# Performance work log

Hardware: AMD Instinct MI355X
Metric: run time of the kernel (lower is better)

## Reference

```python
import jax, jax.numpy as jnp
import numpy as np

NUM_LABELS = 64
START, END, PAD = 0, 1, 2
B, L, V, D = 128, 1024, 30000, 256


def make_transitions(key):
    # replicates CRF.init_weights
    t = jax.random.uniform(key, (NUM_LABELS, NUM_LABELS), minval=-0.1, maxval=0.1)
    t = t.at[:, START].set(-10000.0)
    t = t.at[END, :].set(-10000.0)
    t = t.at[PAD, :].set(-10000.0)
    t = t.at[:, PAD].set(-10000.0)
    t = t.at[PAD, PAD].set(0.0)
    t = t.at[PAD, END].set(0.0)
    return t.astype(jnp.float32)


def setup_inputs() -> dict:
    key = jax.random.key(0)
    k0, k1, k2, k3, k4 = jax.random.split(key, 5)
    x = jax.random.randint(k0, (B, L), 0, V)
    tags = jax.random.randint(k1, (B, L), 0, NUM_LABELS)
    mask = jnp.ones((B, L), dtype=jnp.float32)  # ignored by CRF (source passes mask=None)
    embed = jax.random.normal(k2, (V, D), dtype=jnp.float32)
    W = jax.random.normal(k3, (D, NUM_LABELS), dtype=jnp.float32) * 0.05
    b = jnp.zeros((NUM_LABELS,), dtype=jnp.float32)
    trans = make_transitions(k4)
    return {"x": x, "tags": tags, "mask": mask, "embed": embed, "W": W, "b": b, "trans": trans}


def _crf_nll(emissions, tags, trans):
    # emissions: [B, L, T]; tags: [B, L]; trans: [T, T]
    # NOTE: original CRF.forward ignores the user mask (passes mask=None ->
    # all-ones mask), so every position is valid and last tag is tags[:, -1].
    # gold path score
    e_scores = jnp.take_along_axis(emissions, tags[:, :, None], axis=2)[:, :, 0].sum(axis=1)
    t_scores = trans[tags[:, :-1], tags[:, 1:]].sum(axis=1)
    scores = e_scores + t_scores + trans[START, tags[:, 0]] + trans[tags[:, -1], END]
    # log partition: forward algorithm (log-space recursion over time)
    alpha0 = trans[START][None, :] + emissions[:, 0]  # [B, T]

    def step(alphas, emit_t):
        # alphas: [B, T_prev] -> logsumexp over previous tag
        new = jax.nn.logsumexp(alphas[:, :, None] + trans[None, :, :], axis=1) + emit_t
        return new, None

    alphas, _ = jax.lax.scan(step, alpha0, jnp.swapaxes(emissions[:, 1:], 0, 1))
    log_z = jax.nn.logsumexp(alphas + trans[:, END][None, :], axis=1)  # [B]
    return -jnp.sum(scores - log_z)


def reference(x, tags, mask, embed, W, b, trans):
    emissions = embed[x] @ W + b  # [B, L, T]
    return _crf_nll(emissions, tags, trans)
```

## Files before the change

kernel.cpp:

```cpp
#include <hip/hip_runtime.h>
#include <hip/hip_bf16.h>

#define B_ 128
#define L_ 1024
#define T_ 64
#define CSH 5
#define C_ 32

using short8 = __attribute__((ext_vector_type(8))) short;
using f32x4  = __attribute__((ext_vector_type(4))) float;
using f32x16 = __attribute__((ext_vector_type(16))) float;

static __device__ __forceinline__ unsigned short bfb(float x) {
  return __builtin_bit_cast(unsigned short, __float2bfloat16(x));
}
static __device__ __forceinline__ float asf(unsigned u) { return __builtin_bit_cast(float, u); }
static __device__ __forceinline__ float bf2f(unsigned short b) { return asf(((unsigned)b) << 16); }
static __device__ __forceinline__ unsigned pk2(float lo, float hi) {
  __hip_bfloat162 h = __float22bfloat162_rn(float2{lo, hi});
  unsigned u;
  __builtin_memcpy(&u, &h, 4);
  return u;
}
static __device__ __forceinline__ unsigned pk2t(float lo, float hi) {
  return __builtin_amdgcn_perm(__builtin_bit_cast(unsigned, hi),
                               __builtin_bit_cast(unsigned, lo), 0x07060302u);
}
static __device__ __forceinline__ void pswap(unsigned& x, unsigned& y) {
  asm("v_permlane32_swap_b32 %0, %1" : "+v"(x), "+v"(y));
}

__global__ __launch_bounds__(256) void k_prep(const float* __restrict__ W,
                                              unsigned short* __restrict__ Wswz,
                                              float* __restrict__ out) {
  if (blockIdx.x == 0 && threadIdx.x == 0) out[0] = 0.f;
  const int t = blockIdx.x * 256 + threadIdx.x;
  const int e = t * 4, k = e >> 6, n0 = e & 63;
  float4 w4 = *(const float4*)(W + e);
  const int base = ((k >> 5) << 11) + ((n0 >> 4) << 9) + (((k >> 3) & 3) << 7) +
                   ((n0 & 15) << 3) + (k & 7);
  Wswz[base + 0]  = bfb(w4.x);
  Wswz[base + 8]  = bfb(w4.y);
  Wswz[base + 16] = bfb(w4.z);
  Wswz[base + 24] = bfb(w4.w);
}

__global__ __launch_bounds__(256) void k_scan(const int* __restrict__ x,
                                              const int* __restrict__ tags,
                                              const float* __restrict__ embed,
                                              const unsigned short* __restrict__ Wswz,
                                              const float* __restrict__ bias,
                                              const float* __restrict__ trans,
                                              unsigned short* __restrict__ XT,
                                              float* __restrict__ rlog,
                                              float* __restrict__ goldF) {
  __shared__ __align__(16) unsigned short Ftile[4][2048];
  const int wv = threadIdx.x >> 6, L = threadIdx.x & 63;
  const int job = blockIdx.x * 4 + wv;
  const int c = job & (C_ - 1);
  const int b = job >> CSH;
  const int K = (1023 + C_ - 1) >> CSH;
  const int a = 1 + c * K;
  const int len = min(K, 1024 - a);
  const int nh = L & 31, hh = L >> 5;
  const int m = L & 15, q = L >> 4;
  unsigned short* Ft = Ftile[wv];

  const float bj0 = bias[m], bj1 = bias[16 + m], bj2 = bias[32 + m], bj3 = bias[48 + m];
  for (int p = 0; p < 2; p++) {
    int tok = a + 16 * p + m;
    if (tok > 1023) tok = 1023;
    const float* er = embed + (size_t)x[b * 1024 + tok] * 256;
    f32x4 acc[4] = {{0.f,0.f,0.f,0.f},{0.f,0.f,0.f,0.f},{0.f,0.f,0.f,0.f},{0.f,0.f,0.f,0.f}};
#pragma unroll
    for (int kap = 0; kap < 8; kap++) {
      float4 p0 = *(const float4*)(er + 32 * kap + 8 * q);
      float4 p1 = *(const float4*)(er + 32 * kap + 8 * q + 4);
      unsigned u0 = pk2(p0.x, p0.y), u1 = pk2(p0.z, p0.w);
      unsigned u2 = pk2(p1.x, p1.y), u3 = pk2(p1.z, p1.w);
      short8 af = __builtin_bit_cast(short8, make_uint4(u0, u1, u2, u3));
#pragma unroll
      for (int u = 0; u < 4; u++) {
        short8 bf8 = *(const short8*)&Wswz[kap * 2048 + u * 512 + q * 128 + m * 8];
        acc[u] = __builtin_amdgcn_mfma_f32_16x16x32_bf16(af, bf8, acc[u], 0, 0, 0);
      }
    }
#pragma unroll
    for (int r = 0; r < 4; r++) {
      float e0 = acc[0][r] + bj0, e1 = acc[1][r] + bj1;
      float e2 = acc[2][r] + bj2, e3 = acc[3][r] + bj3;
      float mr = fmaxf(fmaxf(e0, e1), fmaxf(e2, e3));
#pragma unroll
      for (int off = 1; off < 16; off <<= 1) mr = fmaxf(mr, __shfl_xor(mr, off));
      float x0 = __expf(e0 - mr), x1 = __expf(e1 - mr);
      float x2 = __expf(e2 - mr), x3 = __expf(e3 - mr);
      float sr = (x0 + x1) + (x2 + x3);
#pragma unroll
      for (int off = 1; off < 16; off <<= 1) sr += __shfl_xor(sr, off);
      float rs = 1.0f / sr;
      const int row = 16 * p + 4 * q + r;
      Ft[row * 64 + m]      = bfb(x0 * rs);
      Ft[row * 64 + 16 + m] = bfb(x1 * rs);
      Ft[row * 64 + 32 + m] = bfb(x2 * rs);
      Ft[row * 64 + 48 + m] = bfb(x3 * rs);
    }
  }
  if (L < len) {
    const int tgv = tags[b * 1024 + a + L];
    goldF[b * 1024 + a + L] = __logf(bf2f(Ft[L * 64 + tgv]));
  }

  short8 Af[2][4];
#pragma unroll
  for (int I = 0; I < 2; I++)
#pragma unroll
    for (int kap = 0; kap < 4; kap++) {
      short8 aa;
#pragma unroll
      for (int d = 0; d < 8; d++) {
        const int k = 16 * kap + 8 * hh + d;
        aa[d] = (short)bfb(__expf(trans[k * T_ + 32 * I + nh]));
      }
      Af[I][kap] = aa;
    }

  unsigned Bf[4][2][4];
#pragma unroll
  for (int kap = 0; kap < 4; kap++)
#pragma unroll
    for (int J = 0; J < 2; J++)
#pragma unroll
      for (int dw = 0; dw < 4; dw++) {
        int k0 = 16 * kap + 8 * hh + 2 * dw, n = 32 * J + nh;
        unsigned u = 0;
        if (k0 == n) u = 0x3F80u;
        if (k0 + 1 == n) u = 0x3F800000u;
        Bf[kap][J][dw] = u;
      }

  float logacc = 0.f;
  const f32x16 Z = {};

  for (int s = 0; s < len; s++) {
    uint2 Fc[2][4];
#pragma unroll
    for (int I = 0; I < 2; I++)
#pragma unroll
      for (int j = 0; j < 4; j++)
        Fc[I][j] = *(const uint2*)&Ft[s * 64 + (16 * I + 4 * j + 2 * hh) * 2];
    const bool rn = ((s & 15) == 15);
    float rs = 1.0f;
#pragma unroll
    for (int J = 0; J < 2; J++) {
      f32x16 D[2];
#pragma unroll
      for (int I = 0; I < 2; I++) {
        short8 b0 = __builtin_bit_cast(short8,
            make_uint4(Bf[0][J][0], Bf[0][J][1], Bf[0][J][2], Bf[0][J][3]));
        f32x16 d = __builtin_amdgcn_mfma_f32_32x32x16_bf16(Af[I][0], b0, Z, 0, 0, 0);
#pragma unroll
        for (int kap = 1; kap < 4; kap++) {
          short8 bk = __builtin_bit_cast(short8,
              make_uint4(Bf[kap][J][0], Bf[kap][J][1], Bf[kap][J][2], Bf[kap][J][3]));
          d = __builtin_amdgcn_mfma_f32_32x32x16_bf16(Af[I][kap], bk, d, 0, 0, 0);
        }
        D[I] = d;
      }
#pragma unroll
      for (int I = 0; I < 2; I++)
#pragma unroll
        for (int j = 0; j < 4; j++) {
          uint2 g = Fc[I][j];
          float f0 = asf(g.x << 16), f1 = asf(g.x & 0xffff0000u);
          float f2 = asf(g.y << 16), f3 = asf(g.y & 0xffff0000u);
          D[I][4 * j + 0] *= f0;
          D[I][4 * j + 1] *= f1;
          D[I][4 * j + 2] *= f2;
          D[I][4 * j + 3] *= f3;
        }
      if (rn) {
        if (J == 0) {
          float mx = D[0][0];
#pragma unroll
          for (int I = 0; I < 2; I++)
#pragma unroll
            for (int r = 0; r < 16; r++) mx = fmaxf(mx, D[I][r]);
#pragma unroll
          for (int off = 1; off < 64; off <<= 1) mx = fmaxf(mx, __shfl_xor(mx, off));
          rs = 1.0f / mx;
          logacc += __logf(mx);
        }
#pragma unroll
        for (int I = 0; I < 2; I++)
#pragma unroll
          for (int r = 0; r < 16; r++) D[I][r] *= rs;
      }
      unsigned PDt[2][4][2];
#pragma unroll
      for (int I = 0; I < 2; I++)
#pragma unroll
        for (int j = 0; j < 4; j++) {
          PDt[I][j][0] = pk2t(D[I][4 * j + 0], D[I][4 * j + 1]);
          PDt[I][j][1] = pk2t(D[I][4 * j + 2], D[I][4 * j + 3]);
        }
      if (s == len - 1) {
        unsigned short* Xrow = XT + (size_t)job * 4096 + 32 * J + nh;
#pragma unroll
        for (int I = 0; I < 2; I++)
#pragma unroll
          for (int j = 0; j < 4; j++)
#pragma unroll
            for (int pp = 0; pp < 2; pp++) {
              const int r = 32 * I + 8 * j + 4 * hh + 2 * pp;
              Xrow[(size_t)r * 64] = (unsigned short)(PDt[I][j][pp] & 0xffffu);
              Xrow[(size_t)(r + 1) * 64] = (unsigned short)(PDt[I][j][pp] >> 16);
            }
      } else {
#pragma unroll
        for (int kap = 0; kap < 4; kap++) {
          const int Ip = kap >> 1, e2 = 2 * (kap & 1);
          unsigned x0 = PDt[Ip][e2][0], y0 = PDt[Ip][e2 + 1][0];
          unsigned x1 = PDt[Ip][e2][1], y1 = PDt[Ip][e2 + 1][1];
          pswap(x0, y0);
          pswap(x1, y1);
          Bf[kap][J][0] = x0;
          Bf[kap][J][1] = x1;
          Bf[kap][J][2] = y0;
          Bf[kap][J][3] = y1;
        }
      }
    }
  }
  if (L == 0) rlog[job] = logacc;
}

__global__ __launch_bounds__(256) void k_apply(const unsigned short* __restrict__ XT,
                                               const float* __restrict__ rlog,
                                               const float* __restrict__ goldF,
                                               const int* __restrict__ x,
                                               const float* __restrict__ embed,
                                               const float* __restrict__ W,
                                               const float* __restrict__ bias,
                                               const float* __restrict__ trans,
                                               const int* __restrict__ tags,
                                               float* __restrict__ out) {
  const int b = blockIdx.x, tid = threadIdx.x;
  __shared__ float sred[4];
  __shared__ __align__(16) float vS[64];
  const int* tg = tags + (size_t)b * L_;
  float acc = 0.f;
  for (int l = tid; l < L_; l += 256) {
    if (l > 0) acc += goldF[(size_t)b * L_ + l];
    if (l < L_ - 1) acc += trans[tg[l] * T_ + tg[l + 1]];
  }
#pragma unroll
  for (int off = 32; off > 0; off >>= 1) acc += __shfl_xor(acc, off);
  if ((tid & 63) == 0) sred[tid >> 6] = acc;
  __syncthreads();
  if (tid >= 64) return;
  const int i = tid;
  float score = (sred[0] + sred[1]) + (sred[2] + sred[3]);
  const float* er0 = embed + (size_t)x[(size_t)b * L_] * 256;
  float e = bias[i];
#pragma unroll 8
  for (int d = 0; d < 256; d++) e = fmaf(er0[d], W[d * T_ + i], e);
  float mr = e;
#pragma unroll
  for (int off = 1; off < 64; off <<= 1) mr = fmaxf(mr, __shfl_xor(mr, off));
  float pex = __expf(e - mr);
  float sr = pex;
#pragma unroll
  for (int off = 1; off < 64; off <<= 1) sr += __shfl_xor(sr, off);
  const int t0 = tg[0];
  score += (__shfl(e, t0) - mr) - __logf(sr);
  score += trans[t0] + trans[tg[L_ - 1] * T_ + 1];
  float v = __expf(trans[i]) * (pex / sr);
  float lacc = 0.f;
  vS[i] = v;
  const uint4* Xb = (const uint4*)XT + (size_t)b * C_ * 512;
  uint4 Xr[8];
#pragma unroll
  for (int t = 0; t < 8; t++) Xr[t] = Xb[i * 8 + t];
  for (int c = 0; c < C_; c++) {
    uint4 Xn[8];
    if (c + 1 < C_) {
#pragma unroll
      for (int t = 0; t < 8; t++) Xn[t] = Xb[(size_t)(c + 1) * 512 + i * 8 + t];
    }
    float nv = 0.f;
#pragma unroll
    for (int t = 0; t < 8; t++) {
      float4 va = *(const float4*)&vS[8 * t];
      float4 vb = *(const float4*)&vS[8 * t + 4];
      nv = fmaf(asf(Xr[t].x << 16), va.x, nv);
      nv = fmaf(asf(Xr[t].x & 0xffff0000u), va.y, nv);
      nv = fmaf(asf(Xr[t].y << 16), va.z, nv);
      nv = fmaf(asf(Xr[t].y & 0xffff0000u), va.w, nv);
      nv = fmaf(asf(Xr[t].z << 16), vb.x, nv);
      nv = fmaf(asf(Xr[t].z & 0xffff0000u), vb.y, nv);
      nv = fmaf(asf(Xr[t].w << 16), vb.z, nv);
      nv = fmaf(asf(Xr[t].w & 0xffff0000u), vb.w, nv);
    }
    float mx = nv;
#pragma unroll
    for (int off = 1; off < 64; off <<= 1) mx = fmaxf(mx, __shfl_xor(mx, off));
    v = nv * (1.0f / mx);
    lacc += __logf(mx) + rlog[b * C_ + c];
    vS[i] = v;
#pragma unroll
    for (int t = 0; t < 8; t++) Xr[t] = Xn[t];
  }
  float t2 = v * __expf(trans[i * T_ + 1]);
#pragma unroll
  for (int off = 1; off < 64; off <<= 1) t2 += __shfl_xor(t2, off);
  if (i == 0) {
    const float logz = lacc + __logf(t2);
    atomicAdd(out, -(score - logz));
  }
}

extern "C" void kernel_launch(void* const* d_in, const int* in_sizes, int n_in,
                              void* d_out, int out_size, void* d_ws, size_t ws_size,
                              hipStream_t stream) {
  const int* x = (const int*)d_in[0];
  const int* tags = (const int*)d_in[1];
  const float* embed = (const float*)d_in[3];
  const float* W = (const float*)d_in[4];
  const float* bias = (const float*)d_in[5];
  const float* trans = (const float*)d_in[6];

  char* ws = (char*)d_ws;
  unsigned short* XT = (unsigned short*)ws;
  float* rlog = (float*)(ws + (size_t)C_ * 1048576);
  float* goldF = (float*)((char*)rlog + (size_t)128 * C_ * 4);
  unsigned short* Wswz = (unsigned short*)((char*)goldF + (size_t)B_ * L_ * 4);
  float* out = (float*)d_out;

  k_prep<<<16, 256, 0, stream>>>(W, Wswz, out);
  k_scan<<<32 * C_, 256, 0, stream>>>(x, tags, embed, Wswz, bias, trans, XT, rlog, goldF);
  k_apply<<<B_, 256, 0, stream>>>(XT, rlog, goldF, x, embed, W, bias, trans, tags, out);
}
```

Before: 203.0 us.

## Fuse apply stage into scan kernel via last-block-done counter

Removes the separate k_apply launch. Each scan wave now reduces its gold emission and transition scores and adds them with an atomic into a per-batch score. The last of the 8 blocks for a batch, detected with an atomic counter, then runs the chunk-combination pass. This drops a kernel launch and the goldF round-trip through memory. In exchange the combine work runs serialized at the tail of whichever block finishes last, and it relies on threadfence ordering. It also splits the dot-product accumulators into four chains to shorten dependency latency.

Result: slower. 266.4 us (+31.2%).

```diff
diff --git a/kernel.cpp b/kernel.cpp
--- a/kernel.cpp
+++ b/kernel.cpp
@@ -32,8 +32,14 @@
 
 __global__ __launch_bounds__(256) void k_prep(const float* __restrict__ W,
                                               unsigned short* __restrict__ Wswz,
+                                              float* __restrict__ score,
+                                              unsigned* __restrict__ cnt,
                                               float* __restrict__ out) {
-  if (blockIdx.x == 0 && threadIdx.x == 0) out[0] = 0.f;
+  if (blockIdx.x == 0) {
+    if (threadIdx.x < 128) score[threadIdx.x] = 0.f;
+    else cnt[threadIdx.x - 128] = 0u;
+    if (threadIdx.x == 0) out[0] = 0.f;
+  }
   const int t = blockIdx.x * 256 + threadIdx.x;
   const int e = t * 4, k = e >> 6, n0 = e & 63;
   float4 w4 = *(const float4*)(W + e);
@@ -49,12 +55,17 @@
                                               const int* __restrict__ tags,
                                               const float* __restrict__ embed,
                                               const unsigned short* __restrict__ Wswz,
+                                              const float* __restrict__ W,
                                               const float* __restrict__ bias,
                                               const float* __restrict__ trans,
                                               unsigned short* __restrict__ XT,
                                               float* __restrict__ rlog,
-                                              float* __restrict__ goldF) {
+                                              float* __restrict__ score,
+                                              unsigned* __restrict__ cnt,
+                                              float* __restrict__ out) {
   __shared__ __align__(16) unsigned short Ftile[4][2048];
+  __shared__ __align__(16) float vS[64];
+  __shared__ int isTail;
   const int wv = threadIdx.x >> 6, L = threadIdx.x & 63;
   const int job = blockIdx.x * 4 + wv;
   const int c = job & (C_ - 1);
@@ -65,6 +76,7 @@
   const int nh = L & 31, hh = L >> 5;
   const int m = L & 15, q = L >> 4;
   unsigned short* Ft = Ftile[wv];
+  const int* tg = tags + (size_t)b * L_;
 
   const float bj0 = bias[m], bj1 = bias[16 + m], bj2 = bias[32 + m], bj3 = bias[48 + m];
   for (int p = 0; p < 2; p++) {
@@ -105,9 +117,15 @@
       Ft[row * 64 + 48 + m] = bfb(x3 * rs);
     }
   }
-  if (L < len) {
-    const int tgv = tags[b * 1024 + a + L];
-    goldF[b * 1024 + a + L] = __logf(bf2f(Ft[L * 64 + tgv]));
+  {
+    float gold = 0.f;
+    if (L < len) {
+      const int tga = tg[a + L], tgp = tg[a - 1 + L];
+      gold = __logf(bf2f(Ft[L * 64 + tga])) + trans[tgp * T_ + tga];
+    }
+#pragma unroll
+    for (int off = 1; off < 64; off <<= 1) gold += __shfl_xor(gold, off);
+    if (L == 0) atomicAdd(&score[b], gold);
   }
 
   short8 Af[2][4];
@@ -123,7 +141,6 @@
       }
       Af[I][kap] = aa;
     }
-
   unsigned Bf[4][2][4];
 #pragma unroll
   for (int kap = 0; kap < 4; kap++)
@@ -140,7 +157,6 @@
 
   float logacc = 0.f;
   const f32x16 Z = {};
-
   for (int s = 0; s < len; s++) {
     uint2 Fc[2][4];
 #pragma unroll
@@ -232,38 +248,28 @@
     }
   }
   if (L == 0) rlog[job] = logacc;
-}
-
-__global__ __launch_bounds__(256) void k_apply(const unsigned short* __restrict__ XT,
-                                               const float* __restrict__ rlog,
-                                               const float* __restrict__ goldF,
-                                               const int* __restrict__ x,
-                                               const float* __restrict__ embed,
-                                               const float* __restrict__ W,
-                                               const float* __restrict__ bias,
-                                               const float* __restrict__ trans,
-                                               const int* __restrict__ tags,
-                                               float* __restrict__ out) {
-  const int b = blockIdx.x, tid = threadIdx.x;
-  __shared__ float sred[4];
-  __shared__ __align__(16) float vS[64];
-  const int* tg = tags + (size_t)b * L_;
-  float acc = 0.f;
-  for (int l = tid; l < L_; l += 256) {
-    if (l > 0) acc += goldF[(size_t)b * L_ + l];
-    if (l < L_ - 1) acc += trans[tg[l] * T_ + tg[l + 1]];
-  }
-#pragma unroll
-  for (int off = 32; off > 0; off >>= 1) acc += __shfl_xor(acc, off);
-  if ((tid & 63) == 0) sred[tid >> 6] = acc;
+
   __syncthreads();
-  if (tid >= 64) return;
-  const int i = tid;
-  float score = (sred[0] + sred[1]) + (sred[2] + sred[3]);
+  if (threadIdx.x == 0) {
+    __threadfence();
+    unsigned old = atomicAdd(&cnt[b], 1u);
+    isTail = (old == 7u);
+  }
+  __syncthreads();
+  if (!isTail || threadIdx.x >= 64) return;
+
+  __threadfence();
+  const int i = L;
   const float* er0 = embed + (size_t)x[(size_t)b * L_] * 256;
-  float e = bias[i];
-#pragma unroll 8
-  for (int d = 0; d < 256; d++) e = fmaf(er0[d], W[d * T_ + i], e);
+  float e0 = bias[i], e1 = 0.f, e2 = 0.f, e3 = 0.f;
+#pragma unroll 16
+  for (int d = 0; d < 256; d += 4) {
+    e0 = fmaf(er0[d + 0], W[(d + 0) * T_ + i], e0);
+    e1 = fmaf(er0[d + 1], W[(d + 1) * T_ + i], e1);
+    e2 = fmaf(er0[d + 2], W[(d + 2) * T_ + i], e2);
+    e3 = fmaf(er0[d + 3], W[(d + 3) * T_ + i], e3);
+  }
+  float e = (e0 + e1) + (e2 + e3);
   float mr = e;
 #pragma unroll
   for (int off = 1; off < 64; off <<= 1) mr = fmaxf(mr, __shfl_xor(mr, off));
@@ -272,8 +278,9 @@
 #pragma unroll
   for (int off = 1; off < 64; off <<= 1) sr += __shfl_xor(sr, off);
   const int t0 = tg[0];
-  score += (__shfl(e, t0) - mr) - __logf(sr);
-  score += trans[t0] + trans[tg[L_ - 1] * T_ + 1];
+  float sc = score[b];
+  sc += (__shfl(e, t0) - mr) - __logf(sr);
+  sc += trans[t0] + trans[tg[L_ - 1] * T_ + 1];
   float v = __expf(trans[i]) * (pex / sr);
   float lacc = 0.f;
   vS[i] = v;
@@ -281,31 +288,32 @@
   uint4 Xr[8];
 #pragma unroll
   for (int t = 0; t < 8; t++) Xr[t] = Xb[i * 8 + t];
-  for (int c = 0; c < C_; c++) {
+  for (int cc = 0; cc < C_; cc++) {
     uint4 Xn[8];
-    if (c + 1 < C_) {
-#pragma unroll
-      for (int t = 0; t < 8; t++) Xn[t] = Xb[(size_t)(c + 1) * 512 + i * 8 + t];
-    }
-    float nv = 0.f;
+    if (cc + 1 < C_) {
+#pragma unroll
+      for (int t = 0; t < 8; t++) Xn[t] = Xb[(size_t)(cc + 1) * 512 + i * 8 + t];
+    }
+    float a0 = 0.f, a1 = 0.f, a2 = 0.f, a3 = 0.f;
 #pragma unroll
     for (int t = 0; t < 8; t++) {
       float4 va = *(const float4*)&vS[8 * t];
       float4 vb = *(const float4*)&vS[8 * t + 4];
-      nv = fmaf(asf(Xr[t].x << 16), va.x, nv);
-      nv = fmaf(asf(Xr[t].x & 0xffff0000u), va.y, nv);
-      nv = fmaf(asf(Xr[t].y << 16), va.z, nv);
-      nv = fmaf(asf(Xr[t].y & 0xffff0000u), va.w, nv);
-      nv = fmaf(asf(Xr[t].z << 16), vb.x, nv);
-      nv = fmaf(asf(Xr[t].z & 0xffff0000u), vb.y, nv);
-      nv = fmaf(asf(Xr[t].w << 16), vb.z, nv);
-      nv = fmaf(asf(Xr[t].w & 0xffff0000u), vb.w, nv);
-    }
+      a0 = fmaf(asf(Xr[t].x << 16), va.x, a0);
+      a1 = fmaf(asf(Xr[t].x & 0xffff0000u), va.y, a1);
+      a2 = fmaf(asf(Xr[t].y << 16), va.z, a2);
+      a3 = fmaf(asf(Xr[t].y & 0xffff0000u), va.w, a3);
+      a0 = fmaf(asf(Xr[t].z << 16), vb.x, a0);
+      a1 = fmaf(asf(Xr[t].z & 0xffff0000u), vb.y, a1);
+      a2 = fmaf(asf(Xr[t].w << 16), vb.z, a2);
+      a3 = fmaf(asf(Xr[t].w & 0xffff0000u), vb.w, a3);
+    }
+    float nv = (a0 + a1) + (a2 + a3);
     float mx = nv;
 #pragma unroll
     for (int off = 1; off < 64; off <<= 1) mx = fmaxf(mx, __shfl_xor(mx, off));
     v = nv * (1.0f / mx);
-    lacc += __logf(mx) + rlog[b * C_ + c];
+    lacc += __logf(mx) + rlog[b * C_ + cc];
     vS[i] = v;
 #pragma unroll
     for (int t = 0; t < 8; t++) Xr[t] = Xn[t];
@@ -315,7 +323,7 @@
   for (int off = 1; off < 64; off <<= 1) t2 += __shfl_xor(t2, off);
   if (i == 0) {
     const float logz = lacc + __logf(t2);
-    atomicAdd(out, -(score - logz));
+    atomicAdd(out, -(sc - logz));
   }
 }
 
@@ -332,11 +340,12 @@
   char* ws = (char*)d_ws;
   unsigned short* XT = (unsigned short*)ws;
   float* rlog = (float*)(ws + (size_t)C_ * 1048576);
-  float* goldF = (float*)((char*)rlog + (size_t)128 * C_ * 4);
-  unsigned short* Wswz = (unsigned short*)((char*)goldF + (size_t)B_ * L_ * 4);
+  float* score = (float*)((char*)rlog + 4096 * 4);
+  unsigned* cnt = (unsigned*)((char*)score + 128 * 4);
+  unsigned short* Wswz = (unsigned short*)((char*)cnt + 128 * 4);
   float* out = (float*)d_out;
 
-  k_prep<<<16, 256, 0, stream>>>(W, Wswz, out);
-  k_scan<<<32 * C_, 256, 0, stream>>>(x, tags, embed, Wswz, bias, trans, XT, rlog, goldF);
-  k_apply<<<B_, 256, 0, stream>>>(XT, rlog, goldF, x, embed, W, bias, trans, tags, out);
-}
+  k_prep<<<16, 256, 0, stream>>>(W, Wswz, score, cnt, out);
+  k_scan<<<32 * C_, 256, 0, stream>>>(x, tags, embed, Wswz, W, bias, trans,
+                                      XT, rlog, score, cnt, out);
+}
```

## Combine chunk transfer matrices via parallel MFMA tree reduction before apply

Applied to the files above, without the earlier changes.

Adds a k_comb kernel that multiplies the per-chunk 64x64 transfer matrices together on MFMA units. It runs as two levels (4-way, then 8-way) and rescales the product by its max, accumulating the log scale into clog. k_apply then does a single matvec with the combined matrix, replacing its 32-step sequential chain of matvec plus max-reduction per batch. The cost is two extra kernel launches and extra bf16 rounding on the matrix products. The first-emission dot product in k_apply is also split into four accumulators.

Result: faster. 197.5 us (-2.7%).

```diff
diff --git a/kernel.cpp b/kernel.cpp
--- a/kernel.cpp
+++ b/kernel.cpp
@@ -32,8 +32,12 @@
 
 __global__ __launch_bounds__(256) void k_prep(const float* __restrict__ W,
                                               unsigned short* __restrict__ Wswz,
+                                              float* __restrict__ clog,
                                               float* __restrict__ out) {
-  if (blockIdx.x == 0 && threadIdx.x == 0) out[0] = 0.f;
+  if (blockIdx.x == 0) {
+    if (threadIdx.x < 128) clog[threadIdx.x] = 0.f;
+    if (threadIdx.x == 0) out[0] = 0.f;
+  }
   const int t = blockIdx.x * 256 + threadIdx.x;
   const int e = t * 4, k = e >> 6, n0 = e & 63;
   float4 w4 = *(const float4*)(W + e);
@@ -123,7 +127,6 @@
       }
       Af[I][kap] = aa;
     }
-
   unsigned Bf[4][2][4];
 #pragma unroll
   for (int kap = 0; kap < 4; kap++)
@@ -140,7 +143,6 @@
 
   float logacc = 0.f;
   const f32x16 Z = {};
-
   for (int s = 0; s < len; s++) {
     uint2 Fc[2][4];
 #pragma unroll
@@ -234,8 +236,115 @@
   if (L == 0) rlog[job] = logacc;
 }
 
-__global__ __launch_bounds__(256) void k_apply(const unsigned short* __restrict__ XT,
+__global__ __launch_bounds__(256) void k_comb(const unsigned short* __restrict__ src,
+                                              unsigned short* __restrict__ dst,
+                                              float* __restrict__ clog,
+                                              int rounds, int outPerBatch) {
+  const int wv = threadIdx.x >> 6, L = threadIdx.x & 63;
+  const int job = blockIdx.x * 4 + wv;
+  const int b = job / outPerBatch;
+  const int nh = L & 31, hh = L >> 5;
+  const unsigned short* S0 = src + (size_t)job * rounds * 4096;
+
+  unsigned Bf[4][2][4];
+#pragma unroll
+  for (int kap = 0; kap < 4; kap++)
+#pragma unroll
+    for (int J = 0; J < 2; J++)
+#pragma unroll
+      for (int dw = 0; dw < 4; dw++) {
+        int k0 = 16 * kap + 8 * hh + 2 * dw, n = 32 * J + nh;
+        unsigned u = 0;
+        if (k0 == n) u = 0x3F80u;
+        if (k0 + 1 == n) u = 0x3F800000u;
+        Bf[kap][J][dw] = u;
+      }
+
+  const f32x16 Z = {};
+  float rs = 1.0f;
+  for (int r = 0; r < rounds; r++) {
+    short8 Af[2][4];
+#pragma unroll
+    for (int I = 0; I < 2; I++)
+#pragma unroll
+      for (int kap = 0; kap < 4; kap++)
+        Af[I][kap] = *(const short8*)(S0 + (size_t)r * 4096 +
+                                      (32 * I + nh) * 64 + 16 * kap + 8 * hh);
+    const bool last = (r == rounds - 1);
+#pragma unroll
+    for (int J = 0; J < 2; J++) {
+      f32x16 D[2];
+#pragma unroll
+      for (int I = 0; I < 2; I++) {
+        short8 b0 = __builtin_bit_cast(short8,
+            make_uint4(Bf[0][J][0], Bf[0][J][1], Bf[0][J][2], Bf[0][J][3]));
+        f32x16 d = __builtin_amdgcn_mfma_f32_32x32x16_bf16(Af[I][0], b0, Z, 0, 0, 0);
+#pragma unroll
+        for (int kap = 1; kap < 4; kap++) {
+          short8 bk = __builtin_bit_cast(short8,
+              make_uint4(Bf[kap][J][0], Bf[kap][J][1], Bf[kap][J][2], Bf[kap][J][3]));
+          d = __builtin_amdgcn_mfma_f32_32x32x16_bf16(Af[I][kap], bk, d, 0, 0, 0);
+        }
+        D[I] = d;
+      }
+      if (last) {
+        if (J == 0) {
+          float mx = D[0][0];
+#pragma unroll
+          for (int I = 0; I < 2; I++)
+#pragma unroll
+            for (int rr = 0; rr < 16; rr++) mx = fmaxf(mx, D[I][rr]);
+#pragma unroll
+          for (int off = 1; off < 64; off <<= 1) mx = fmaxf(mx, __shfl_xor(mx, off));
+          rs = 1.0f / mx;
+          if (L == 0) atomicAdd(&clog[b], __logf(mx));
+        }
+#pragma unroll
+        for (int I = 0; I < 2; I++)
+#pragma unroll
+          for (int rr = 0; rr < 16; rr++) D[I][rr] *= rs;
+      }
+      unsigned PDt[2][4][2];
+#pragma unroll
+      for (int I = 0; I < 2; I++)
+#pragma unroll
+        for (int j = 0; j < 4; j++) {
+          PDt[I][j][0] = pk2t(D[I][4 * j + 0], D[I][4 * j + 1]);
+          PDt[I][j][1] = pk2t(D[I][4 * j + 2], D[I][4 * j + 3]);
+        }
+      if (last) {
+        unsigned short* Xrow = dst + (size_t)job * 4096 + 32 * J + nh;
+#pragma unroll
+        for (int I = 0; I < 2; I++)
+#pragma unroll
+          for (int j = 0; j < 4; j++)
+#pragma unroll
+            for (int pp = 0; pp < 2; pp++) {
+              const int rr = 32 * I + 8 * j + 4 * hh + 2 * pp;
+              Xrow[(size_t)rr * 64] = (unsigned short)(PDt[I][j][pp] & 0xffffu);
+              Xrow[(size_t)(rr + 1) * 64] = (unsigned short)(PDt[I][j][pp] >> 16);
+            }
+      } else {
+#pragma unroll
+        for (int kap = 0; kap < 4; kap++) {
+          const int Ip = kap >> 1, e2 = 2 * (kap & 1);
+          unsigned x0 = PDt[Ip][e2][0], y0 = PDt[Ip][e2 + 1][0];
+          unsigned x1 = PDt[Ip][e2][1], y1 = PDt[Ip][e2 + 1][1];
+          pswap(x0, y0);
+          pswap(x1, y1);
+          Bf[kap][J][0] = x0;
+          Bf[kap][J][1] = x1;
+          Bf[kap][J][2] = y0;
+          Bf[kap][J][3] = y1;
+        }
+      }
+    }
+  }
+}
+
+__global__ __launch_bounds__(256) void k_apply(const unsigned short* __restrict__ Zm,
                                                const float* __restrict__ rlog,
+                                               const float* __restrict__ clog,
                                                const float* __restrict__ goldF,
                                                const int* __restrict__ x,
                                                const float* __restrict__ embed,
@@ -261,9 +370,15 @@
   const int i = tid;
   float score = (sred[0] + sred[1]) + (sred[2] + sred[3]);
   const float* er0 = embed + (size_t)x[(size_t)b * L_] * 256;
-  float e = bias[i];
-#pragma unroll 8
-  for (int d = 0; d < 256; d++) e = fmaf(er0[d], W[d * T_ + i], e);
+  float e0 = bias[i], e1 = 0.f, e2 = 0.f, e3 = 0.f;
+#pragma unroll 16
+  for (int d = 0; d < 256; d += 4) {
+    e0 = fmaf(er0[d + 0], W[(d + 0) * T_ + i], e0);
+    e1 = fmaf(er0[d + 1], W[(d + 1) * T_ + i], e1);
+    e2 = fmaf(er0[d + 2], W[(d + 2) * T_ + i], e2);
+    e3 = fmaf(er0[d + 3], W[(d + 3) * T_ + i], e3);
+  }
+  float e = (e0 + e1) + (e2 + e3);
   float mr = e;
 #pragma unroll
   for (int off = 1; off < 64; off <<= 1) mr = fmaxf(mr, __shfl_xor(mr, off));
@@ -275,46 +390,33 @@
   score += (__shfl(e, t0) - mr) - __logf(sr);
   score += trans[t0] + trans[tg[L_ - 1] * T_ + 1];
   float v = __expf(trans[i]) * (pex / sr);
-  float lacc = 0.f;
   vS[i] = v;
-  const uint4* Xb = (const uint4*)XT + (size_t)b * C_ * 512;
+  float rl = (i < 32) ? rlog[b * C_ + i] : 0.f;
+#pragma unroll
+  for (int off = 1; off < 64; off <<= 1) rl += __shfl_xor(rl, off);
+  const uint4* Zr = (const uint4*)(Zm + (size_t)b * 4096);
   uint4 Xr[8];
 #pragma unroll
-  for (int t = 0; t < 8; t++) Xr[t] = Xb[i * 8 + t];
-  for (int c = 0; c < C_; c++) {
-    uint4 Xn[8];
-    if (c + 1 < C_) {
-#pragma unroll
-      for (int t = 0; t < 8; t++) Xn[t] = Xb[(size_t)(c + 1) * 512 + i * 8 + t];
-    }
-    float nv = 0.f;
-#pragma unroll
-    for (int t = 0; t < 8; t++) {
-      float4 va = *(const float4*)&vS[8 * t];
-      float4 vb = *(const float4*)&vS[8 * t + 4];
-      nv = fmaf(asf(Xr[t].x << 16), va.x, nv);
-      nv = fmaf(asf(Xr[t].x & 0xffff0000u), va.y, nv);
-      nv = fmaf(asf(Xr[t].y << 16), va.z, nv);
-      nv = fmaf(asf(Xr[t].y & 0xffff0000u), va.w, nv);
-      nv = fmaf(asf(Xr[t].z << 16), vb.x, nv);
-      nv = fmaf(asf(Xr[t].z & 0xffff0000u), vb.y, nv);
-      nv = fmaf(asf(Xr[t].w << 16), vb.z, nv);
-      nv = fmaf(asf(Xr[t].w & 0xffff0000u), vb.w, nv);
-    }
-    float mx = nv;
-#pragma unroll
-    for (int off = 1; off < 64; off <<= 1) mx = fmaxf(mx, __shfl_xor(mx, off));
-    v = nv * (1.0f / mx);
-    lacc += __logf(mx) + rlog[b * C_ + c];
-    vS[i] = v;
-#pragma unroll
-    for (int t = 0; t < 8; t++) Xr[t] = Xn[t];
-  }
-  float t2 = v * __expf(trans[i * T_ + 1]);
+  for (int t = 0; t < 8; t++) Xr[t] = Zr[i * 8 + t];
+  float a0 = 0.f, a1 = 0.f, a2 = 0.f, a3 = 0.f;
+#pragma unroll
+  for (int t = 0; t < 8; t++) {
+    float4 va = *(const float4*)&vS[8 * t];
+    float4 vb = *(const float4*)&vS[8 * t + 4];
+    a0 = fmaf(asf(Xr[t].x << 16), va.x, a0);
+    a1 = fmaf(asf(Xr[t].x & 0xffff0000u), va.y, a1);
+    a2 = fmaf(asf(Xr[t].y << 16), va.z, a2);
+    a3 = fmaf(asf(Xr[t].y & 0xffff0000u), va.w, a3);
+    a0 = fmaf(asf(Xr[t].z << 16), vb.x, a0);
+    a1 = fmaf(asf(Xr[t].z & 0xffff0000u), vb.y, a1);
+    a2 = fmaf(asf(Xr[t].w << 16), vb.z, a2);
+    a3 = fmaf(asf(Xr[t].w & 0xffff0000u), vb.w, a3);
+  }
+  float t2 = ((a0 + a1) + (a2 + a3)) * __expf(trans[i * T_ + 1]);
 #pragma unroll
   for (int off = 1; off < 64; off <<= 1) t2 += __shfl_xor(t2, off);
   if (i == 0) {
-    const float logz = lacc + __logf(t2);
+    const float logz = clog[b] + rl + __logf(t2);
     atomicAdd(out, -(score - logz));
   }
 }
@@ -331,12 +433,18 @@
 
   char* ws = (char*)d_ws;
   unsigned short* XT = (unsigned short*)ws;
-  float* rlog = (float*)(ws + (size_t)C_ * 1048576);
-  float* goldF = (float*)((char*)rlog + (size_t)128 * C_ * 4);
-  unsigned short* Wswz = (unsigned short*)((char*)goldF + (size_t)B_ * L_ * 4);
+  unsigned short* Y  = (unsigned short*)(ws + 33554432);
+  unsigned short* Zm = (unsigned short*)(ws + 33554432 + 8388608);
+  char* tail = ws + 33554432 + 8388608 + 1048576;
+  float* rlog = (float*)tail;
+  float* goldF = (float*)(tail + 16384);
+  float* clog = (float*)(tail + 16384 + 524288);
+  unsigned short* Wswz = (unsigned short*)(tail + 16384 + 524288 + 512);
   float* out = (float*)d_out;
 
-  k_prep<<<16, 256, 0, stream>>>(W, Wswz, out);
+  k_prep<<<16, 256, 0, stream>>>(W, Wswz, clog, out);
   k_scan<<<32 * C_, 256, 0, stream>>>(x, tags, embed, Wswz, bias, trans, XT, rlog, goldF);
-  k_apply<<<B_, 256, 0, stream>>>(XT, rlog, goldF, x, embed, W, bias, trans, tags, out);
-}
+  k_comb<<<256, 256, 0, stream>>>(XT, Y, clog, 4, 8);
+  k_comb<<<32, 256, 0, stream>>>(Y, Zm, clog, 8, 1);
+  k_apply<<<B_, 256, 0, stream>>>(Zm, rlog, clog, goldF, x, embed, W, bias, trans, tags, out);
+}
```
